# Kernel tuning notes

Measured on AMD Instinct MI355X. Metric: run time of the kernel, lower is better.

Reference implementation:

```python
import jax, jax.numpy as jnp
import numpy as np

B, N, C = 64, 197, 768
H, GH, D = 12, 2, 64           # num_heads, global_heads, head_dim
HR = H // GH                    # head_ratio = 6
TOTAL_HEADS = 2 * GH + H        # 16
SCALE = D ** -0.5
LEVELS = 3


def setup_inputs() -> dict:
    key = jax.random.key(0)
    ks = jax.random.split(key, 10)
    s = 0.02
    return {
        "x": jax.random.normal(ks[0], (B, N, C), jnp.float32),
        "qkv_w": jax.random.normal(ks[1], (C, TOTAL_HEADS * D), jnp.float32) * s,
        "qkv_b": jax.random.normal(ks[2], (TOTAL_HEADS * D,), jnp.float32) * s,
        "masks": jax.random.uniform(ks[3], (N, N, LEVELS), jnp.float32),
        "mask_proj": jnp.ones((LEVELS, H), jnp.float32),
        "mask_base": jax.random.normal(ks[4], (H,), jnp.float32) * s,
        "head_proj_w": jnp.eye(H, dtype=jnp.float32) + jax.random.normal(ks[5], (H, H), jnp.float32) * s,
        "head_proj_b": jax.random.normal(ks[6], (H,), jnp.float32) * s,
        "proj_w": jax.random.normal(ks[7], (C, C), jnp.float32) * s,
        "proj_b": jax.random.normal(ks[8], (C,), jnp.float32) * s,
    }


def reference(x, qkv_w, qkv_b, masks, mask_proj, mask_base, head_proj_w, head_proj_b, proj_w, proj_b):
    b, n, c = x.shape
    # fused qkv projection -> (b, total_heads, n, d)
    qkv = (x @ qkv_w + qkv_b).reshape(b, n, TOTAL_HEADS, D).transpose(0, 2, 1, 3)
    q = qkv[:, :GH]                 # (b, gh, n, d)
    k = qkv[:, GH:2 * GH]           # (b, gh, n, d)
    v = qkv[:, 2 * GH:]             # (b, h, n, d)

    # global-head attention scores (b, gh, n, n)
    attn = jnp.einsum("bgnd,bgmd->bgnm", q, k) * SCALE

    # per-pair learned mask weights: (n, n, levels) @ (levels, h) -> (n, n, h)
    mw = masks @ mask_proj + mask_base
    # reshape to (1, gh, n, n, hr) per global_proj_type='full'
    mw = mw.reshape(n, n, GH, HR).transpose(2, 0, 1, 3)[None]

    # modulate scores: (b, gh, n, n, hr)
    a = attn[..., None] * mw

    # non_linear head mixing: relu then per-position linear over heads
    a = a.transpose(0, 2, 3, 1, 4).reshape(b, n, n, H)   # (b, n, n, h)
    a = jax.nn.relu(a) @ head_proj_w + head_proj_b
    a = a.transpose(0, 3, 1, 2)                          # (b, h, n, n)

    a = jax.nn.softmax(a, axis=-1)
    out = jnp.einsum("bhnm,bhmd->bnhd", a, v).reshape(b, n, c)
    return out @ proj_w + proj_b
```

## Files before the change

### kernel.cpp

```cpp
#include <hip/hip_runtime.h>
#include <cstdint>
#include <cstddef>

#define BB   64
#define NN   197
#define CC   768
#define HH   12
#define THD  16
#define DD   64
#define MROWS (BB*NN)
#define QKVN (THD*DD)
#define SCALE_ 0.125f
#define ATTS 208
#define KPAD 224
#define SSTR 240

typedef unsigned short u16;
typedef __attribute__((ext_vector_type(2))) float f32x2;
typedef __attribute__((ext_vector_type(4))) float f32x4;
typedef __attribute__((ext_vector_type(8))) short s16x8;
typedef __attribute__((address_space(1))) unsigned int as1_u32;
typedef __attribute__((address_space(3))) unsigned int as3_u32;

__device__ __forceinline__ float bf2f(u16 u) {
  union { unsigned int i; float f; } x; x.i = ((unsigned int)u) << 16; return x.f;
}
__device__ __forceinline__ u16 f2bf(float f) {
  unsigned int x = __builtin_bit_cast(unsigned int, f);
  unsigned int r = (x + 0x7fffu + ((x >> 16) & 1u)) >> 16;
  return (u16)r;
}
__device__ __forceinline__ void gl_lds16(const u16* g, u16* l) {
  __builtin_amdgcn_global_load_lds((const as1_u32*)g, (as3_u32*)l, 16, 0, 0);
}

__global__ __launch_bounds__(256) void k_cvt_x(const float* __restrict__ src,
                                               u16* __restrict__ dst, int n8) {
  int i = blockIdx.x * 256 + threadIdx.x;
  if (i >= n8) return;
  const float4* s = (const float4*)src;
  float4 a = s[2 * i], b = s[2 * i + 1];
  ushort4 lo, hi;
  lo.x = f2bf(a.x); lo.y = f2bf(a.y); lo.z = f2bf(a.z); lo.w = f2bf(a.w);
  hi.x = f2bf(b.x); hi.y = f2bf(b.y); hi.z = f2bf(b.z); hi.w = f2bf(b.w);
  ((ushort4*)dst)[2 * i] = lo;
  ((ushort4*)dst)[2 * i + 1] = hi;
}

__global__ __launch_bounds__(256) void k_transpose(const float* __restrict__ in,
                                                   u16* __restrict__ out,
                                                   int R, int Ccol) {
  __shared__ u16 tile[32][33];
  int c0 = blockIdx.x * 32, r0 = blockIdx.y * 32;
  int tx = threadIdx.x & 31, ty = threadIdx.x >> 5;
#pragma unroll
  for (int i = 0; i < 32; i += 8) {
    int r = r0 + ty + i, c = c0 + tx;
    tile[ty + i][tx] = (r < R && c < Ccol) ? f2bf(in[(size_t)r * Ccol + c]) : (u16)0;
  }
  __syncthreads();
#pragma unroll
  for (int i = 0; i < 32; i += 8) {
    int cc = c0 + ty + i, rr = r0 + tx;
    if (cc < Ccol && rr < R) out[(size_t)cc * R + rr] = tile[tx][ty + i];
  }
}

__global__ __launch_bounds__(256, 3) void k_gemm_bt(const u16* __restrict__ A,
                                                    const u16* __restrict__ Bt,
                                                    const float* __restrict__ bias,
                                                    void* __restrict__ Cout,
                                                    int M, int Nn, int K,
                                                    int write_bf16) {
  __shared__ u16 SHG[24576];
  u16* As = SHG;
  u16* Bs = SHG + 12288;
  int t = threadIdx.x;
  int w = t >> 6, lane = t & 63;

  int NT = gridDim.y;
  int nwg = gridDim.x * gridDim.y;
  int d = blockIdx.y * gridDim.x + blockIdx.x;
  int q8 = nwg >> 3, r8 = nwg & 7;
  int xcd = d & 7, j = d >> 3;
  int g = (xcd < r8 ? xcd * (q8 + 1) : r8 * (q8 + 1) + (xcd - r8) * q8) + j;
  int mt = g / NT, nt_ = g - mt * NT;
  int m0 = mt * 128, n0 = nt_ * 128;

  int wm = w >> 1, wn = w & 1;

  f32x4 acc[4][4];
#pragma unroll
  for (int i = 0; i < 4; i++)
#pragma unroll
    for (int j2 = 0; j2 < 4; j2++)
#pragma unroll
      for (int e = 0; e < 4; e++) acc[i][j2][e] = 0.f;

  int lrow4 = lane >> 2;
  int lkc = (lane & 3) * 8;

  auto stage = [&](int buf, int kk) {
#pragma unroll
    for (int rc = 0; rc < 2; rc++) {
      int c = w + rc * 4;
      int row = c * 16 + lrow4;
      int ga = m0 + row; if (ga >= M) ga = M - 1;
      gl_lds16(A + (size_t)ga * K + kk + lkc, &As[buf * 4096 + c * 512]);
      gl_lds16(Bt + (size_t)(n0 + row) * K + kk + lkc, &Bs[buf * 4096 + c * 512]);
    }
  };

  auto compute = [&](int buf) {
    int r16 = lane & 15, k8 = (lane >> 4) * 8;
    s16x8 af[4], bfv[4];
#pragma unroll
    for (int s = 0; s < 4; s++) {
      af[s]  = *(const s16x8*)&As[buf * 4096 + (wm * 64 + s * 16 + r16) * 32 + k8];
      bfv[s] = *(const s16x8*)&Bs[buf * 4096 + (wn * 64 + s * 16 + r16) * 32 + k8];
    }
#pragma unroll
    for (int sm = 0; sm < 4; sm++)
#pragma unroll
      for (int sn = 0; sn < 4; sn++)
        acc[sm][sn] = __builtin_amdgcn_mfma_f32_16x16x32_bf16(af[sm], bfv[sn], acc[sm][sn], 0, 0, 0);
  };

  int nt = K >> 5;
  stage(0, 0);
  stage(1, 32);
  for (int tt = 0; tt < nt - 2; ++tt) {
    stage((tt + 2) % 3, (tt + 2) * 32);
    asm volatile("s_waitcnt vmcnt(8)" ::: "memory");
    __builtin_amdgcn_sched_barrier(0);
    __builtin_amdgcn_s_barrier();
    compute(tt % 3);
    __builtin_amdgcn_s_barrier();
  }
  asm volatile("s_waitcnt vmcnt(4)" ::: "memory");
  __builtin_amdgcn_sched_barrier(0);
  __builtin_amdgcn_s_barrier();
  compute((nt - 2) % 3);
  __builtin_amdgcn_s_barrier();
  asm volatile("s_waitcnt vmcnt(0)" ::: "memory");
  __builtin_amdgcn_sched_barrier(0);
  __builtin_amdgcn_s_barrier();
  compute((nt - 1) % 3);

  int quad = lane >> 4, col = lane & 15;
  if (write_bf16) {
    u16* Cb = (u16*)Cout;
    u16* O = SHG;
    __syncthreads();
#pragma unroll
    for (int sn = 0; sn < 4; sn++) {
      int gn = n0 + wn * 64 + sn * 16 + col;
      float bv = bias[gn];
#pragma unroll
      for (int sm = 0; sm < 4; sm++)
#pragma unroll
        for (int i = 0; i < 4; i++)
          O[(wm * 64 + sm * 16 + quad * 4 + i) * 136 + wn * 64 + sn * 16 + col] =
              f2bf(acc[sm][sn][i] + bv);
    }
    __syncthreads();
#pragma unroll
    for (int it = 0; it < 8; it++) {
      int q = t + it * 256;
      int rl = q >> 4, c8 = q & 15;
      int gm = m0 + rl;
      if (gm < M) {
        s16x8 v = *(const s16x8*)&O[rl * 136 + c8 * 8];
        *(s16x8*)&Cb[(size_t)gm * Nn + n0 + c8 * 8] = v;
      }
    }
  } else {
    float* Cf = (float*)Cout;
#pragma unroll
    for (int sn = 0; sn < 4; sn++) {
      int gn = n0 + wn * 64 + sn * 16 + col;
      float bv = bias[gn];
#pragma unroll
      for (int sm = 0; sm < 4; sm++) {
        int gmb = m0 + wm * 64 + sm * 16 + quad * 4;
#pragma unroll
        for (int i = 0; i < 4; i++) {
          int gm = gmb + i;
          if (gm < M) Cf[(size_t)gm * Nn + gn] = acc[sm][sn][i] + bv;
        }
      }
    }
  }
}

__global__ __launch_bounds__(256) void k_qk(const u16* __restrict__ qkv,
                                            float* __restrict__ att) {
  __shared__ u16 As[2][128 * 32];
  __shared__ u16 Bs[2][128 * 32];
  int t = threadIdx.x;
  int w = t >> 6, lane = t & 63;
  int bz = blockIdx.z, b = bz >> 1, g = bz & 1;
  int n0 = blockIdx.x * 128;
  int m0 = blockIdx.y * 128;
  int wm = w >> 1, wn = w & 1;

  f32x4 acc[4][4];
#pragma unroll
  for (int i = 0; i < 4; i++)
#pragma unroll
    for (int j = 0; j < 4; j++)
#pragma unroll
      for (int e = 0; e < 4; e++) acc[i][j][e] = 0.f;

  int lrow4 = lane >> 2, lkc = (lane & 3) * 8;

#pragma unroll
  for (int half = 0; half < 2; half++) {
    int kk = half * 32;
#pragma unroll
    for (int rc = 0; rc < 2; rc++) {
      int c = w + rc * 4;
      int row = c * 16 + lrow4;
      int nq = n0 + row; if (nq > NN - 1) nq = NN - 1;
      int mk = m0 + row; if (mk > NN - 1) mk = NN - 1;
      gl_lds16(qkv + (size_t)(b * NN + nq) * QKVN + g * DD + kk + lkc, &As[half][c * 512]);
      gl_lds16(qkv + (size_t)(b * NN + mk) * QKVN + 2 * DD + g * DD + kk + lkc, &Bs[half][c * 512]);
    }
  }
  __syncthreads();
  {
    int r16 = lane & 15, k8 = (lane >> 4) * 8;
#pragma unroll
    for (int half = 0; half < 2; half++) {
      s16x8 af[4], bfv[4];
#pragma unroll
      for (int s = 0; s < 4; s++) {
        af[s]  = *(const s16x8*)&As[half][(wm * 64 + s * 16 + r16) * 32 + k8];
        bfv[s] = *(const s16x8*)&Bs[half][(wn * 64 + s * 16 + r16) * 32 + k8];
      }
#pragma unroll
      for (int sm = 0; sm < 4; sm++)
#pragma unroll
        for (int sn = 0; sn < 4; sn++)
          acc[sm][sn] = __builtin_amdgcn_mfma_f32_16x16x32_bf16(af[sm], bfv[sn], acc[sm][sn], 0, 0, 0);
    }
  }
  int quad = lane >> 4, col = lane & 15;
#pragma unroll
  for (int sn = 0; sn < 4; sn++) {
    int gn = m0 + wn * 64 + sn * 16 + col;
#pragma unroll
    for (int sm = 0; sm < 4; sm++) {
      int gmb = n0 + wm * 64 + sm * 16 + quad * 4;
#pragma unroll
      for (int i = 0; i < 4; i++) {
        int gm = gmb + i;
        if (gm < NN && gn < NN)
          att[((size_t)bz * NN + gm) * ATTS + gn] = acc[sm][sn][i] * SCALE_;
      }
    }
  }
}

__global__ __launch_bounds__(256) void k_softmax_p(const float* __restrict__ att,
                                                   const float* __restrict__ masks,
                                                   const float* __restrict__ mproj,
                                                   const float* __restrict__ mbase,
                                                   const float* __restrict__ hpw,
                                                   const float* __restrict__ hpb,
                                                   u16* __restrict__ P) {
  __shared__ float S[12][SSTR];
  __shared__ f32x2 hpw_s[72];
  __shared__ f32x2 mp_s[18];
  __shared__ f32x2 mb_s[6], hpb_s[6];
  __shared__ float inv_s[12];
  int t = threadIdx.x;
  int n = blockIdx.x, b = blockIdx.y;

  if (t < 72) hpw_s[t] = ((const f32x2*)hpw)[t];
  if (t < 18) mp_s[t] = ((const f32x2*)mproj)[t];
  if (t < 6) { mb_s[t] = ((const f32x2*)mbase)[t]; hpb_s[t] = ((const f32x2*)hpb)[t]; }
  __syncthreads();

  if (t < NN) {
    int m = t;
    float a0 = att[((size_t)(b * 2 + 0) * NN + n) * ATTS + m];
    float a1 = att[((size_t)(b * 2 + 1) * NN + n) * ATTS + m];
    const float* mk = masks + ((size_t)n * NN + m) * 3;
    float l0 = mk[0], l1 = mk[1], l2 = mk[2];
    f32x2 pre2[6];
#pragma unroll
    for (int k = 0; k < 6; k++) {
      f32x2 wv = mb_s[k] + l0 * mp_s[k] + l1 * mp_s[6 + k] + l2 * mp_s[12 + k];
      float av = (k < 3) ? a0 : a1;
      f32x2 v = wv * av;
      pre2[k].x = v.x > 0.f ? v.x : 0.f;
      pre2[k].y = v.y > 0.f ? v.y : 0.f;
    }
    f32x2 s2[6];
#pragma unroll
    for (int k = 0; k < 6; k++) s2[k] = hpb_s[k];
#pragma unroll
    for (int h = 0; h < 12; h++) {
      float p = (h & 1) ? pre2[h >> 1].y : pre2[h >> 1].x;
#pragma unroll
      for (int k = 0; k < 6; k++) s2[k] += p * hpw_s[h * 6 + k];
    }
#pragma unroll
    for (int k = 0; k < 6; k++) {
      S[2 * k][m] = s2[k].x;
      S[2 * k + 1][m] = s2[k].y;
    }
  } else if (t < KPAD) {
#pragma unroll
    for (int h = 0; h < 12; h++) S[h][t] = 0.f;
  }
  __syncthreads();

  {
    int g = t >> 4, l16 = t & 15;
    if (g < 12) {
      float vals[13];
      float mx = -1e30f;
#pragma unroll
      for (int i = 0; i < 13; i++) {
        int m = l16 + i * 16;
        float x = S[g][m];
        vals[i] = (m < NN) ? x : -1e30f;
        mx = fmaxf(mx, vals[i]);
      }
#pragma unroll
      for (int off = 8; off; off >>= 1) mx = fmaxf(mx, __shfl_xor(mx, off, 16));
      float sum = 0.f;
#pragma unroll
      for (int i = 0; i < 13; i++) {
        int m = l16 + i * 16;
        float e = __expf(vals[i] - mx);
        if (m < NN) { S[g][m] = e; sum += e; }
      }
#pragma unroll
      for (int off = 8; off; off >>= 1) sum += __shfl_xor(sum, off, 16);
      if (l16 == 0) inv_s[g] = 1.f / sum;
    }
  }
  __syncthreads();

  for (int c4 = t; c4 < 672; c4 += 256) {
    int h = c4 / 56;
    int m = (c4 - h * 56) * 4;
    f32x4 v = *(const f32x4*)&S[h][m];
    float iv = inv_s[h];
    ushort4 u;
    u.x = f2bf(v.x * iv); u.y = f2bf(v.y * iv);
    u.z = f2bf(v.z * iv); u.w = f2bf(v.w * iv);
    *(ushort4*)(P + ((size_t)(b * HH + h) * NN + n) * KPAD + m) = u;
  }
}

__global__ __launch_bounds__(256) void k_pv(const u16* __restrict__ P,
                                            const u16* __restrict__ qkv,
                                            u16* __restrict__ aout) {
  __shared__ u16 SH[18432];
  u16* As = SH;
  u16* Bs = SH + 14336;
  int t = threadIdx.x;
  int w = t >> 6, lane = t & 63;
  int bh = blockIdx.x, b = bh / HH, h = bh - b * HH;

  f32x4 acc[4][4];
#pragma unroll
  for (int i = 0; i < 4; i++)
#pragma unroll
    for (int j = 0; j < 4; j++)
#pragma unroll
      for (int e = 0; e < 4; e++) acc[i][j][e] = 0.f;

  int lrow4 = lane >> 2, lkc = (lane & 3) * 8;
  int vml = t & 31, vd0 = (t >> 5) * 8;

  for (int k0 = 0; k0 < KPAD; k0 += 64) {
    int nh = (KPAD - k0 >= 64) ? 2 : 1;
    for (int half = 0; half < nh; half++) {
      int kk = k0 + half * 32;
#pragma unroll
      for (int rc = 0; rc < 4; rc++) {
        int c = w + rc * 4;
        if (c < 14) {
          int row = c * 16 + lrow4;
          int gn = row > NN - 1 ? NN - 1 : row;
          gl_lds16(P + ((size_t)bh * NN + gn) * KPAD + kk + lkc, &As[half * 7168 + c * 512]);
        }
      }
      {
        int m = kk + vml;
        u16 v8[8];
        if (m < NN) {
          const ushort4* vp = (const ushort4*)(qkv + (size_t)(b * NN + m) * QKVN + (4 + h) * DD + vd0);
          ushort4 lo = vp[0], hi = vp[1];
          v8[0] = lo.x; v8[1] = lo.y; v8[2] = lo.z; v8[3] = lo.w;
          v8[4] = hi.x; v8[5] = hi.y; v8[6] = hi.z; v8[7] = hi.w;
        } else {
#pragma unroll
          for (int j = 0; j < 8; j++) v8[j] = 0;
        }
#pragma unroll
        for (int j = 0; j < 8; j++) Bs[half * 2048 + (vd0 + j) * 32 + vml] = v8[j];
      }
    }
    __syncthreads();
    int r16 = lane & 15, k8 = (lane >> 4) * 8;
    for (int half = 0; half < nh; half++) {
      s16x8 bfv[4];
#pragma unroll
      for (int s = 0; s < 4; s++)
        bfv[s] = *(const s16x8*)&Bs[half * 2048 + (s * 16 + r16) * 32 + k8];
#pragma unroll
      for (int si = 0; si < 4; si++) {
        int smt = w + si * 4;
        if (smt < 14) {
          s16x8 af = *(const s16x8*)&As[half * 7168 + (smt * 16 + r16) * 32 + k8];
#pragma unroll
          for (int sn = 0; sn < 4; sn++)
            acc[si][sn] = __builtin_amdgcn_mfma_f32_16x16x32_bf16(af, bfv[sn], acc[si][sn], 0, 0, 0);
        }
      }
    }
    __syncthreads();
  }

  int quad = lane >> 4, col = lane & 15;
  u16* O = SH;
#pragma unroll
  for (int si = 0; si < 4; si++) {
    int smt = w + si * 4;
    if (smt < 14) {
#pragma unroll
      for (int sn = 0; sn < 4; sn++)
#pragma unroll
        for (int i = 0; i < 4; i++)
          O[(smt * 16 + quad * 4 + i) * 80 + sn * 16 + col] = f2bf(acc[si][sn][i]);
    }
  }
  __syncthreads();
  for (int q = t; q < NN * 8; q += 256) {
    int rl = q >> 3, c8 = q & 7;
    s16x8 v = *(const s16x8*)&O[rl * 80 + c8 * 8];
    *(s16x8*)&aout[(size_t)(b * NN + rl) * CC + h * DD + c8 * 8] = v;
  }
}

extern "C" void kernel_launch(void* const* d_in, const int* in_sizes, int n_in,
                              void* d_out, int out_size, void* d_ws, size_t ws_size,
                              hipStream_t stream) {
  const float* x     = (const float*)d_in[0];
  const float* qkv_w = (const float*)d_in[1];
  const float* qkv_b = (const float*)d_in[2];
  const float* masks = (const float*)d_in[3];
  const float* mproj = (const float*)d_in[4];
  const float* mbase = (const float*)d_in[5];
  const float* hpw   = (const float*)d_in[6];
  const float* hpb   = (const float*)d_in[7];
  const float* projw = (const float*)d_in[8];
  const float* projb = (const float*)d_in[9];

  char* ws = (char*)d_ws;
  size_t off = 0;
  auto alloc = [&](size_t bytes) {
    char* p = ws + off; off = (off + bytes + 255) & ~(size_t)255; return p;
  };
  char*  r1   = alloc((size_t)BB * 2 * NN * ATTS * 4);
  u16*   xbf  = (u16*)r1;
  float* att  = (float*)r1;
  u16*   aout = (u16*)r1;
  u16*   qkv  = (u16*)alloc((size_t)MROWS * QKVN * 2);
  u16*   P    = (u16*)alloc((size_t)BB * HH * NN * KPAD * 2);
  u16*   wt1  = (u16*)alloc((size_t)QKVN * CC * 2);
  u16*   wt2  = (u16*)alloc((size_t)CC * CC * 2);

  int n8 = MROWS * CC / 8;
  k_cvt_x<<<(n8 + 255) / 256, 256, 0, stream>>>(x, xbf, n8);
  k_transpose<<<dim3(QKVN / 32, CC / 32), 256, 0, stream>>>(qkv_w, wt1, CC, QKVN);
  k_transpose<<<dim3(CC / 32, CC / 32), 256, 0, stream>>>(projw, wt2, CC, CC);
  k_gemm_bt<<<dim3((MROWS + 127) / 128, QKVN / 128), 256, 0, stream>>>(
      xbf, wt1, qkv_b, qkv, MROWS, QKVN, CC, 1);
  k_qk<<<dim3(2, 2, BB * 2), 256, 0, stream>>>(qkv, att);
  k_softmax_p<<<dim3(NN, BB), 256, 0, stream>>>(att, masks, mproj, mbase, hpw, hpb, P);
  k_pv<<<dim3(BB * HH), 256, 0, stream>>>(P, qkv, aout);
  k_gemm_bt<<<dim3((MROWS + 127) / 128, CC / 128), 256, 0, stream>>>(
      aout, wt2, projb, d_out, MROWS, CC, CC, 0);
}
```

Baseline: 240.5 us.

## Precompute sign-split head-mix weights per position and drop softmax max pass

The score modulation is rewritten using the identity relu(a*w) = a*relu(w) when a>0 and a*min(w,0) otherwise. A new prep kernel precomputes, for each (n,m) pair and each global head, the head-mixed weight vectors for both signs. The softmax kernel then only picks a sign branch and does three vector FMAs per output group, instead of rebuilding mask weights and doing a 12x12 mix per element. It also skips the max-subtraction pass and exponentiates directly, relying on logits staying small. The grid is reordered so blocks sharing the same n run next to each other, which should help cache reuse of the 7.5 MB precomputed table. In exchange, each element reads 24 floats instead of 3, and softmax can overflow for large logits.

Measured after the change: 249.1 us. 3.6% more time.

```diff
diff --git a/kernel.cpp b/kernel.cpp
--- a/kernel.cpp
+++ b/kernel.cpp
@@ -66,6 +66,41 @@
   }
 }
 
+__global__ __launch_bounds__(256) void k_pp(const float* __restrict__ masks,
+                                            const float* __restrict__ mproj,
+                                            const float* __restrict__ mbase,
+                                            const float* __restrict__ hpw,
+                                            float* __restrict__ pp) {
+  int i = blockIdx.x * 256 + threadIdx.x;
+  if (i >= NN * NN) return;
+  float l0 = masks[(size_t)i * 3], l1 = masks[(size_t)i * 3 + 1], l2 = masks[(size_t)i * 3 + 2];
+  f32x4 acc[4][3];
+#pragma unroll
+  for (int s = 0; s < 4; s++)
+#pragma unroll
+    for (int q = 0; q < 3; q++)
+#pragma unroll
+      for (int e = 0; e < 4; e++) acc[s][q][e] = 0.f;
+#pragma unroll
+  for (int h = 0; h < 12; h++) {
+    float w = mbase[h] + l0 * mproj[h] + l1 * mproj[12 + h] + l2 * mproj[24 + h];
+    float wp = fmaxf(w, 0.f), wn = fminf(w, 0.f);
+    int s0 = (h < 6) ? 0 : 2;
+    const f32x4* hw = (const f32x4*)(hpw + h * 12);
+#pragma unroll
+    for (int q = 0; q < 3; q++) {
+      f32x4 hv = hw[q];
+      acc[s0][q]     += wp * hv;
+      acc[s0 + 1][q] += wn * hv;
+    }
+  }
+  f32x4* out = (f32x4*)(pp + (size_t)i * 48);
+#pragma unroll
+  for (int s = 0; s < 4; s++)
+#pragma unroll
+    for (int q = 0; q < 3; q++) out[s * 3 + q] = acc[s][q];
+}
+
 __global__ __launch_bounds__(256, 3) void k_gemm_bt(const u16* __restrict__ A,
                                                     const u16* __restrict__ Bt,
                                                     const float* __restrict__ bias,
@@ -263,53 +298,33 @@
 }
 
 __global__ __launch_bounds__(256) void k_softmax_p(const float* __restrict__ att,
-                                                   const float* __restrict__ masks,
-                                                   const float* __restrict__ mproj,
-                                                   const float* __restrict__ mbase,
-                                                   const float* __restrict__ hpw,
+                                                   const float* __restrict__ pp,
                                                    const float* __restrict__ hpb,
                                                    u16* __restrict__ P) {
   __shared__ float S[12][SSTR];
-  __shared__ f32x2 hpw_s[72];
-  __shared__ f32x2 mp_s[18];
-  __shared__ f32x2 mb_s[6], hpb_s[6];
   __shared__ float inv_s[12];
+  __shared__ f32x4 hpb_s[3];
   int t = threadIdx.x;
-  int n = blockIdx.x, b = blockIdx.y;
-
-  if (t < 72) hpw_s[t] = ((const f32x2*)hpw)[t];
-  if (t < 18) mp_s[t] = ((const f32x2*)mproj)[t];
-  if (t < 6) { mb_s[t] = ((const f32x2*)mbase)[t]; hpb_s[t] = ((const f32x2*)hpb)[t]; }
+  int b = blockIdx.x, n = blockIdx.y;
+
+  if (t < 3) hpb_s[t] = ((const f32x4*)hpb)[t];
   __syncthreads();
 
   if (t < NN) {
     int m = t;
     float a0 = att[((size_t)(b * 2 + 0) * NN + n) * ATTS + m];
     float a1 = att[((size_t)(b * 2 + 1) * NN + n) * ATTS + m];
-    const float* mk = masks + ((size_t)n * NN + m) * 3;
-    float l0 = mk[0], l1 = mk[1], l2 = mk[2];
-    f32x2 pre2[6];
-#pragma unroll
-    for (int k = 0; k < 6; k++) {
-      f32x2 wv = mb_s[k] + l0 * mp_s[k] + l1 * mp_s[6 + k] + l2 * mp_s[12 + k];
-      float av = (k < 3) ? a0 : a1;
-      f32x2 v = wv * av;
-      pre2[k].x = v.x > 0.f ? v.x : 0.f;
-      pre2[k].y = v.y > 0.f ? v.y : 0.f;
-    }
-    f32x2 s2[6];
-#pragma unroll
-    for (int k = 0; k < 6; k++) s2[k] = hpb_s[k];
-#pragma unroll
-    for (int h = 0; h < 12; h++) {
-      float p = (h & 1) ? pre2[h >> 1].y : pre2[h >> 1].x;
-#pragma unroll
-      for (int k = 0; k < 6; k++) s2[k] += p * hpw_s[h * 6 + k];
-    }
-#pragma unroll
-    for (int k = 0; k < 6; k++) {
-      S[2 * k][m] = s2[k].x;
-      S[2 * k + 1][m] = s2[k].y;
+    const float* base = pp + ((size_t)n * NN + m) * 48;
+    const f32x4* p0 = (const f32x4*)(base + (a0 > 0.f ? 0 : 12));
+    const f32x4* p1 = (const f32x4*)(base + (a1 > 0.f ? 24 : 36));
+    f32x4 s0 = hpb_s[0] + a0 * p0[0] + a1 * p1[0];
+    f32x4 s1 = hpb_s[1] + a0 * p0[1] + a1 * p1[1];
+    f32x4 s2 = hpb_s[2] + a0 * p0[2] + a1 * p1[2];
+#pragma unroll
+    for (int k = 0; k < 4; k++) {
+      S[k][m]     = __expf(s0[k]);
+      S[4 + k][m] = __expf(s1[k]);
+      S[8 + k][m] = __expf(s2[k]);
     }
   } else if (t < KPAD) {
 #pragma unroll
@@ -320,24 +335,9 @@
   {
     int g = t >> 4, l16 = t & 15;
     if (g < 12) {
-      float vals[13];
-      float mx = -1e30f;
-#pragma unroll
-      for (int i = 0; i < 13; i++) {
-        int m = l16 + i * 16;
-        float x = S[g][m];
-        vals[i] = (m < NN) ? x : -1e30f;
-        mx = fmaxf(mx, vals[i]);
-      }
-#pragma unroll
-      for (int off = 8; off; off >>= 1) mx = fmaxf(mx, __shfl_xor(mx, off, 16));
       float sum = 0.f;
 #pragma unroll
-      for (int i = 0; i < 13; i++) {
-        int m = l16 + i * 16;
-        float e = __expf(vals[i] - mx);
-        if (m < NN) { S[g][m] = e; sum += e; }
-      }
+      for (int i = 0; i < 13; i++) sum += S[g][l16 + i * 16];
 #pragma unroll
       for (int off = 8; off; off >>= 1) sum += __shfl_xor(sum, off, 16);
       if (l16 == 0) inv_s[g] = 1.f / sum;
@@ -476,15 +476,17 @@
   u16*   P    = (u16*)alloc((size_t)BB * HH * NN * KPAD * 2);
   u16*   wt1  = (u16*)alloc((size_t)QKVN * CC * 2);
   u16*   wt2  = (u16*)alloc((size_t)CC * CC * 2);
+  float* pp   = (float*)alloc((size_t)NN * NN * 48 * 4);
 
   int n8 = MROWS * CC / 8;
   k_cvt_x<<<(n8 + 255) / 256, 256, 0, stream>>>(x, xbf, n8);
   k_transpose<<<dim3(QKVN / 32, CC / 32), 256, 0, stream>>>(qkv_w, wt1, CC, QKVN);
   k_transpose<<<dim3(CC / 32, CC / 32), 256, 0, stream>>>(projw, wt2, CC, CC);
+  k_pp<<<(NN * NN + 255) / 256, 256, 0, stream>>>(masks, mproj, mbase, hpw, pp);
   k_gemm_bt<<<dim3((MROWS + 127) / 128, QKVN / 128), 256, 0, stream>>>(
       xbf, wt1, qkv_b, qkv, MROWS, QKVN, CC, 1);
   k_qk<<<dim3(2, 2, BB * 2), 256, 0, stream>>>(qkv, att);
-  k_softmax_p<<<dim3(NN, BB), 256, 0, stream>>>(att, masks, mproj, mbase, hpw, hpb, P);
+  k_softmax_p<<<dim3(BB, NN), 256, 0, stream>>>(att, pp, hpb, P);
   k_pv<<<dim3(BB * HH), 256, 0, stream>>>(P, qkv, aout);
   k_gemm_bt<<<dim3((MROWS + 127) / 128, CC / 128), 256, 0, stream>>>(
       aout, wt2, projb, d_out, MROWS, CC, CC, 0);
```
